# Kernel optimization log

Hardware: AMD Instinct MI355X
Metric: run time of the kernel (lower is better)

The kernel has to match this reference:

```python
import jax, jax.numpy as jnp
import numpy as np
from jax import lax
from jax.scipy.special import logsumexp

B, S, V, D, DFF, H, T, L = 64, 512, 30000, 128, 256, 4, 9, 2
HD = D // H


def setup_inputs() -> dict:
    key = jax.random.key(0)
    ks = jax.random.split(key, 12)
    sc = 0.02
    return {
        "sentences": jax.random.randint(ks[0], (B, S), 0, V, dtype=jnp.int32),
        "tags": jax.random.randint(ks[1], (B, S), 0, T, dtype=jnp.int32),
        "emb": jax.random.normal(ks[2], (V, D), jnp.float32) * sc,
        "Wqkv": jax.random.normal(ks[3], (L, 3 * D, D), jnp.float32) * sc,
        "bqkv": jnp.zeros((L, 3 * D), jnp.float32),
        "Wo": jax.random.normal(ks[4], (L, D, D), jnp.float32) * sc,
        "bo": jnp.zeros((L, D), jnp.float32),
        "W1": jax.random.normal(ks[5], (L, DFF, D), jnp.float32) * sc,
        "b1f": jnp.zeros((L, DFF), jnp.float32),
        "W2": jax.random.normal(ks[6], (L, D, DFF), jnp.float32) * sc,
        "b2f": jnp.zeros((L, D), jnp.float32),
        "ln1g": jnp.ones((L, D), jnp.float32), "ln1b": jnp.zeros((L, D), jnp.float32),
        "ln2g": jnp.ones((L, D), jnp.float32), "ln2b": jnp.zeros((L, D), jnp.float32),
        "Wtag": jax.random.normal(ks[7], (T, D), jnp.float32) * sc,
        "btag": jnp.zeros((T,), jnp.float32),
        "trans": jax.random.normal(ks[8], (T, T), jnp.float32) * 0.1,
        "start_t": jax.random.normal(ks[9], (T,), jnp.float32),
        "end_t": jax.random.normal(ks[10], (T,), jnp.float32),
    }


def _layernorm(x, g, b, eps=1e-5):
    mu = x.mean(-1, keepdims=True)
    var = ((x - mu) ** 2).mean(-1, keepdims=True)
    return (x - mu) / jnp.sqrt(var + eps) * g + b


def _forward_core(sentences, tags, emb, Wqkv, bqkv, Wo, bo, W1, b1f, W2, b2f,
                  ln1g, ln1b, ln2g, ln2b, Wtag, btag, trans, start_t, end_t):
    emb = emb.at[0].set(0.0)  # padding_idx=0
    mask = sentences != 0  # (B,S) key-padding mask (True = real token)
    x = emb[sentences]  # (B,S,D)
    # sinusoidal positional encoding (eval mode -> dropout is identity)
    pos = jnp.arange(S, dtype=jnp.float32)[:, None]
    div = jnp.exp(jnp.arange(0, D, 2, dtype=jnp.float32) * (-np.log(10000.0) / D))
    pe = jnp.zeros((S, D), jnp.float32).at[:, 0::2].set(jnp.sin(pos * div)).at[:, 1::2].set(jnp.cos(pos * div))
    x = x + pe[None]
    key_bias = jnp.where(mask, 0.0, -1e9)[:, None, None, :]  # (B,1,1,S)
    inv_sqrt_hd = 1.0 / np.sqrt(HD)
    for l in range(L):  # post-LN TransformerEncoderLayer, relu FFN
        qkv = x @ Wqkv[l].T + bqkv[l]
        q, k, v = jnp.split(qkv, 3, axis=-1)
        q = q.reshape(B, S, H, HD)
        k = k.reshape(B, S, H, HD)
        v = v.reshape(B, S, H, HD)
        scores = jnp.einsum('bqhd,bkhd->bhqk', q, k) * inv_sqrt_hd + key_bias
        attn = jax.nn.softmax(scores, axis=-1)
        ctx = jnp.einsum('bhqk,bkhd->bqhd', attn, v).reshape(B, S, D)
        x = _layernorm(x + ctx @ Wo[l].T + bo[l], ln1g[l], ln1b[l])
        ff = jax.nn.relu(x @ W1[l].T + b1f[l]) @ W2[l].T + b2f[l]
        x = _layernorm(x + ff, ln2g[l], ln2b[l])
    emissions = x @ Wtag.T + btag  # (B,S,T)

    # CRF forward algorithm (log-partition) as a scan over time
    fv0 = start_t[None, :] + emissions[:, 0]  # (B,T)

    def step(fv, xm):
        em_t, m_t = xm  # (B,T), (B,)
        nv = logsumexp(fv[:, :, None] + trans[None, :, :] + em_t[:, None, :], axis=1)
        return jnp.where(m_t[:, None], nv, fv), None

    fv, _ = lax.scan(step, fv0, (jnp.swapaxes(emissions[:, 1:], 0, 1),
                                 jnp.swapaxes(mask[:, 1:], 0, 1)))
    fwd_score = logsumexp(fv + end_t[None, :], axis=1)  # (B,)

    # gold path score (fully vectorized)
    bidx = jnp.arange(B)
    score = start_t[tags[:, 0]] + emissions[bidx, 0, tags[:, 0]]
    tprev, tcur = tags[:, :-1], tags[:, 1:]
    trans_sc = trans[tprev, tcur]  # (B,S-1)
    emit_sc = jnp.take_along_axis(emissions[:, 1:], tcur[:, :, None], axis=2)[:, :, 0]
    score = score + jnp.sum(jnp.where(mask[:, 1:], trans_sc + emit_sc, 0.0), axis=1)
    seq_lens = mask.sum(axis=1)
    last_tags = tags[bidx, seq_lens - 1]
    score = score + end_t[last_tags]

    return jnp.mean(fwd_score - score)


def reference(sentences, tags, emb, Wqkv, bqkv, Wo, bo, W1, b1f, W2, b2f,
              ln1g, ln1b, ln2g, ln2b, Wtag, btag, trans, start_t, end_t):
    return _forward_core(sentences, tags, emb, Wqkv, bqkv, Wo, bo, W1, b1f, W2, b2f,
                         ln1g, ln1b, ln2g, ln2b, Wtag, btag, trans, start_t, end_t)
```

## Files before the change

kernel.cpp:

```cpp
#include <hip/hip_runtime.h>
#include <hip/hip_bf16.h>

#define BB   64
#define SS   512
#define DD   128
#define DFFc 256
#define HH   4
#define TT   9
#define LL   2
#define HDc  32
#define NN   (BB*SS)

#define OFF_X    0
#define OFF_Y    (NN*DD)
#define OFF_QKV  (2*NN*DD)
#define OFF_CTX  (5*NN*DD)
#define OFF_KT   (6*NN*DD)
#define OFF_EM   (7*NN*DD)
#define OFF_PART (7*NN*DD + NN*TT)

typedef __attribute__((ext_vector_type(8))) short short8;
typedef __attribute__((ext_vector_type(8))) unsigned short ushort8;
typedef __attribute__((ext_vector_type(4))) float f32x4;

__device__ __forceinline__ unsigned short f2bf(float f) {
  union { __hip_bfloat16 h; unsigned short u; } cv;
  cv.h = __float2bfloat16(f);
  return cv.u;
}
__device__ __forceinline__ float bf2f(unsigned short h) {
  return __uint_as_float(((unsigned int)h) << 16);
}

__global__ void k_embed(const int* __restrict__ sent, const float* __restrict__ emb,
                        float* __restrict__ x,
                        unsigned short* __restrict__ xh, unsigned short* __restrict__ xl) {
  int n = blockIdx.x;
  int d = threadIdx.x;
  int tok = sent[n];
  int s = n & (SS - 1);
  float e = (tok != 0) ? emb[(size_t)tok * DD + d] : 0.f;
  int i = d >> 1;
  float dv = expf((float)(2 * i) * (-9.210340371976184f / (float)DD));
  float ang = (float)s * dv;
  float pe = (d & 1) ? cosf(ang) : sinf(ang);
  float v = e + pe;
  size_t o = (size_t)n * DD + d;
  x[o] = v;
  unsigned short h = f2bf(v);
  xh[o] = h;
  xl[o] = f2bf(v - bf2f(h));
}

__global__ void k_packw(const float* __restrict__ Wqkv, const float* __restrict__ Wo,
                        const float* __restrict__ W1, const float* __restrict__ W2,
                        unsigned short* __restrict__ Wh, unsigned short* __restrict__ Wl) {
  int idx = (blockIdx.x * 256 + threadIdx.x) * 4;
  const float* src;
  int off;
  if (idx < 49152)      { src = Wqkv; off = idx; }
  else if (idx < 65536) { src = Wo;   off = idx - 49152; }
  else if (idx < 98304) { src = W1;   off = idx - 65536; }
  else                  { src = W2;   off = idx - 98304; }
  float4 v = *(const float4*)(src + off);
  unsigned short h0 = f2bf(v.x), h1 = f2bf(v.y), h2 = f2bf(v.z), h3 = f2bf(v.w);
  Wh[idx + 0] = h0; Wh[idx + 1] = h1; Wh[idx + 2] = h2; Wh[idx + 3] = h3;
  Wl[idx + 0] = f2bf(v.x - bf2f(h0));
  Wl[idx + 1] = f2bf(v.y - bf2f(h1));
  Wl[idx + 2] = f2bf(v.z - bf2f(h2));
  Wl[idx + 3] = f2bf(v.w - bf2f(h3));
}

template <int KTOT, bool RELU, bool PACKOUT>
__global__ __launch_bounds__(256) void k_bgemm(
    const unsigned short* __restrict__ Xh, const unsigned short* __restrict__ Xl,
    const unsigned short* __restrict__ Wh, const unsigned short* __restrict__ Wl,
    const float* __restrict__ bias, float* __restrict__ Y, int ldY,
    unsigned short* __restrict__ Yh, unsigned short* __restrict__ Yl,
    int ncb) {
  const int id = blockIdx.x;
  const int cb = id % ncb, rb = id / ncb;
  const int tid = threadIdx.x, w = tid >> 6, lane = tid & 63;
  const int l15 = lane & 15, kg = lane >> 4;
  const int n0 = rb * 64 + w * 16;
  const int c0 = cb * 64;
  f32x4 acc[4] = {};
  const unsigned short* xph = Xh + (size_t)(n0 + l15) * KTOT + kg * 8;
  const unsigned short* xpl = Xl + (size_t)(n0 + l15) * KTOT + kg * 8;
  #pragma unroll
  for (int ks = 0; ks < KTOT / 32; ks++) {
    short8 ah = *(const short8*)(xph + ks * 32);
    short8 al = *(const short8*)(xpl + ks * 32);
    #pragma unroll
    for (int ct = 0; ct < 4; ct++) {
      size_t wo = (size_t)(c0 + ct * 16 + l15) * KTOT + ks * 32 + kg * 8;
      short8 bh = *(const short8*)(Wh + wo);
      short8 bl = *(const short8*)(Wl + wo);
      acc[ct] = __builtin_amdgcn_mfma_f32_16x16x32_bf16(ah, bh, acc[ct], 0, 0, 0);
      acc[ct] = __builtin_amdgcn_mfma_f32_16x16x32_bf16(ah, bl, acc[ct], 0, 0, 0);
      acc[ct] = __builtin_amdgcn_mfma_f32_16x16x32_bf16(al, bh, acc[ct], 0, 0, 0);
    }
  }
  #pragma unroll
  for (int ct = 0; ct < 4; ct++) {
    int c = c0 + ct * 16 + l15;
    float bi = bias[c];
    #pragma unroll
    for (int j = 0; j < 4; j++) {
      float v = acc[ct][j] + bi;
      if (RELU) v = fmaxf(v, 0.f);
      int n = n0 + kg * 4 + j;
      if (PACKOUT) {
        unsigned short h = f2bf(v);
        Yh[(size_t)n * ldY + c] = h;
        Yl[(size_t)n * ldY + c] = f2bf(v - bf2f(h));
      } else {
        Y[(size_t)n * ldY + c] = v;
      }
    }
  }
}

template <int KTOT>
__global__ __launch_bounds__(256) void k_bgemm_ln(
    const unsigned short* __restrict__ Xh, const unsigned short* __restrict__ Xl,
    const unsigned short* __restrict__ Wh, const unsigned short* __restrict__ Wl,
    const float* __restrict__ bias, const float* __restrict__ Res,
    const float* __restrict__ gam, const float* __restrict__ bet,
    float* __restrict__ Y,
    unsigned short* __restrict__ Yh, unsigned short* __restrict__ Yl,
    int dopack) {
  const int tid = threadIdx.x, w = tid >> 6, lane = tid & 63;
  const int l15 = lane & 15, kg = lane >> 4;
  const int n0 = blockIdx.x * 64 + w * 16;
  f32x4 acc[8] = {};
  const unsigned short* xph = Xh + (size_t)(n0 + l15) * KTOT + kg * 8;
  const unsigned short* xpl = Xl + (size_t)(n0 + l15) * KTOT + kg * 8;
  #pragma unroll
  for (int ks = 0; ks < KTOT / 32; ks++) {
    short8 ah = *(const short8*)(xph + ks * 32);
    short8 al = *(const short8*)(xpl + ks * 32);
    #pragma unroll
    for (int ct = 0; ct < 8; ct++) {
      size_t wo = (size_t)(ct * 16 + l15) * KTOT + ks * 32 + kg * 8;
      short8 bh = *(const short8*)(Wh + wo);
      short8 bl = *(const short8*)(Wl + wo);
      acc[ct] = __builtin_amdgcn_mfma_f32_16x16x32_bf16(ah, bh, acc[ct], 0, 0, 0);
      acc[ct] = __builtin_amdgcn_mfma_f32_16x16x32_bf16(ah, bl, acc[ct], 0, 0, 0);
      acc[ct] = __builtin_amdgcn_mfma_f32_16x16x32_bf16(al, bh, acc[ct], 0, 0, 0);
    }
  }
  #pragma unroll
  for (int j = 0; j < 4; j++) {
    int n = n0 + kg * 4 + j;
    float v[8], s1 = 0.f, s2 = 0.f;
    #pragma unroll
    for (int ct = 0; ct < 8; ct++) {
      int c = ct * 16 + l15;
      float t = acc[ct][j] + bias[c] + Res[(size_t)n * DD + c];
      v[ct] = t;
      s1 += t;
      s2 += t * t;
    }
    #pragma unroll
    for (int off = 1; off <= 8; off <<= 1) {
      s1 += __shfl_xor(s1, off);
      s2 += __shfl_xor(s2, off);
    }
    float mu = s1 * 0.0078125f;
    float var = s2 * 0.0078125f - mu * mu;
    float rstd = rsqrtf(var + 1e-5f);
    #pragma unroll
    for (int ct = 0; ct < 8; ct++) {
      int c = ct * 16 + l15;
      float o = (v[ct] - mu) * rstd * gam[c] + bet[c];
      size_t oo = (size_t)n * DD + c;
      Y[oo] = o;
      if (dopack) {
        unsigned short h = f2bf(o);
        Yh[oo] = h;
        Yl[oo] = f2bf(o - bf2f(h));
      }
    }
  }
}

__global__ void k_pack(const float* __restrict__ qkv,
                       unsigned short* __restrict__ Kh, unsigned short* __restrict__ Vh) {
  const int st = blockIdx.x * 64;
  const int bh = blockIdx.y;
  const int b = bh >> 2, h = bh & 3;
  const int tid = threadIdx.x;
  __shared__ float tile[64][33];
  #pragma unroll
  for (int p = 0; p < 8; p++) {
    int sl = p * 8 + (tid >> 5);
    int d = tid & 31;
    const float* src = qkv + (size_t)(b * SS + st + sl) * 384 + h * 32 + d;
    Kh[(size_t)(bh * SS + st + sl) * 32 + d] = f2bf(src[128]);
    tile[sl][d] = src[256];
  }
  __syncthreads();
  int d = tid >> 3, s0 = (tid & 7) * 8;
  ushort8 vh;
  #pragma unroll
  for (int i = 0; i < 8; i++) vh[i] = f2bf(tile[s0 + i][d]);
  *(ushort8*)&Vh[(size_t)(bh * 32 + d) * SS + st + s0] = vh;
}

__global__ __launch_bounds__(256) void k_attn(const float* __restrict__ qkv,
    const unsigned short* __restrict__ Kh, const unsigned short* __restrict__ Vh,
    const int* __restrict__ sent,
    unsigned short* __restrict__ ctxh, unsigned short* __restrict__ ctxl) {
  const int id = blockIdx.x;
  const int xcd = id & 7, rem = id >> 3;
  const int qt = rem & 7;
  const int bh = xcd + 8 * (rem >> 3);
  const int b = bh >> 2, h = bh & 3;
  const int tid = threadIdx.x, w = tid >> 6, lane = tid & 63;
  const int l15 = lane & 15, kg = lane >> 4;

  __shared__ float kb_lds[512];
  __shared__ unsigned short Ph[4][16][136];
  __shared__ float l_lds[4][16];

  for (int i = tid; i < 512; i += 256)
    kb_lds[i] = (sent[b * SS + i] != 0) ? 0.f : -1e9f;
  __syncthreads();

  const int qrow = qt * 64 + w * 16 + l15;
  const float* qp = qkv + (size_t)(b * SS + qrow) * 384 + h * 32 + kg * 8;
  short8 qh;
  #pragma unroll
  for (int i = 0; i < 8; i++) qh[i] = (short)f2bf(qp[i]);

  f32x4 acc0 = {0.f, 0.f, 0.f, 0.f};
  f32x4 acc1 = {0.f, 0.f, 0.f, 0.f};
  float ls[4] = {0.f, 0.f, 0.f, 0.f};
  const float scale = 0.17677669529663687f;

  const unsigned short* KhB = Kh + (size_t)bh * SS * 32;
  const unsigned short* VhB = Vh + (size_t)bh * 32 * SS;

  for (int c = 0; c < 4; c++) {
    const int ksb = c * 128;
    f32x4 sc[8];
    #pragma unroll
    for (int t = 0; t < 8; t++) {
      short8 kh_ = *(const short8*)(KhB + (size_t)(ksb + t * 16 + l15) * 32 + kg * 8);
      f32x4 z = {0.f, 0.f, 0.f, 0.f};
      sc[t] = __builtin_amdgcn_mfma_f32_16x16x32_bf16(qh, kh_, z, 0, 0, 0);
    }
    #pragma unroll
    for (int t = 0; t < 8; t++) {
      float kbv = kb_lds[ksb + t * 16 + l15];
      #pragma unroll
      for (int j = 0; j < 4; j++) {
        float s = fmaf(sc[t][j], scale, kbv);
        float p = __expf(s);
        ls[j] += p;
        Ph[w][kg * 4 + j][t * 16 + l15] = f2bf(p);
      }
    }
    #pragma unroll
    for (int k4 = 0; k4 < 4; k4++) {
      short8 ph_ = *(const short8*)&Ph[w][l15][k4 * 32 + kg * 8];
      short8 vh0 = *(const short8*)(VhB + (size_t)l15 * SS + ksb + k4 * 32 + kg * 8);
      short8 vh1 = *(const short8*)(VhB + (size_t)(16 + l15) * SS + ksb + k4 * 32 + kg * 8);
      acc0 = __builtin_amdgcn_mfma_f32_16x16x32_bf16(vh0, ph_, acc0, 0, 0, 0);
      acc1 = __builtin_amdgcn_mfma_f32_16x16x32_bf16(vh1, ph_, acc1, 0, 0, 0);
    }
  }
  #pragma unroll
  for (int j = 0; j < 4; j++) {
    #pragma unroll
    for (int off = 1; off <= 8; off <<= 1) ls[j] += __shfl_xor(ls[j], off);
  }
  if (l15 == 0) {
    #pragma unroll
    for (int j = 0; j < 4; j++) l_lds[w][kg * 4 + j] = ls[j];
  }
  float linv = 1.f / l_lds[w][l15];
  size_t co = (size_t)(b * SS + qrow) * DD + h * 32;
  #pragma unroll
  for (int j = 0; j < 4; j++) {
    float v0 = acc0[j] * linv;
    float v1 = acc1[j] * linv;
    unsigned short h0 = f2bf(v0), h1 = f2bf(v1);
    ctxh[co + kg * 4 + j] = h0;
    ctxl[co + kg * 4 + j] = f2bf(v0 - bf2f(h0));
    ctxh[co + 16 + kg * 4 + j] = h1;
    ctxl[co + 16 + kg * 4 + j] = f2bf(v1 - bf2f(h1));
  }
}

__global__ void k_emis(const float* __restrict__ X, const float* __restrict__ Wtag,
                       const float* __restrict__ btag, float* __restrict__ em) {
  int idx = blockIdx.x * 256 + threadIdx.x;
  if (idx >= NN * TT) return;
  int n = idx / TT, t = idx - n * TT;
  const float* xr = X + (size_t)n * DD;
  const float* wr = Wtag + (size_t)t * DD;
  float acc = 0.f;
  #pragma unroll
  for (int k = 0; k < DD / 4; k++) {
    float4 x4 = *(const float4*)(xr + 4 * k);
    float4 w4 = *(const float4*)(wr + 4 * k);
    acc += x4.x * w4.x + x4.y * w4.y + x4.z * w4.z + x4.w * w4.w;
  }
  em[idx] = acc + btag[t];
}

__global__ void k_crf_scan(const float* __restrict__ em, const int* __restrict__ sent,
                           const float* __restrict__ trans, float* __restrict__ M) {
  const int i = blockIdx.x;
  const int c = blockIdx.y;
  const int b = blockIdx.z;
  const int lane = threadIdx.x;
  const int j = (lane < TT) ? lane : 0;
  float tr[TT];
  #pragma unroll
  for (int k = 0; k < TT; k++) tr[k] = trans[k * TT + j];
  const float* emb_ = em + (size_t)b * SS * TT;
  float v = (j == i) ? 0.f : -1e30f;
  const int s0 = 1 + c * 64;
  const int s1 = (s0 + 64 < SS) ? s0 + 64 : SS;
  for (int s = s0; s < s1; s++) {
    int tok = sent[b * SS + s];
    if (tok != 0) {
      float a[TT];
      #pragma unroll
      for (int k = 0; k < TT; k++) a[k] = __shfl(v, k) + tr[k];
      float m = a[0];
      #pragma unroll
      for (int k = 1; k < TT; k++) m = fmaxf(m, a[k]);
      float sum = 0.f;
      #pragma unroll
      for (int k = 0; k < TT; k++) sum += __expf(a[k] - m);
      v = emb_[s * TT + j] + m + __logf(sum);
    }
  }
  if (lane < TT) M[(((size_t)b * 8 + c) * TT + i) * TT + j] = v;
}

__global__ void k_crf_comb(const float* __restrict__ em, const int* __restrict__ sent,
                           const int* __restrict__ tags, const float* __restrict__ trans,
                           const float* __restrict__ start_t, const float* __restrict__ end_t,
                           const float* __restrict__ M, float* __restrict__ part) {
  const int b = blockIdx.x;
  const int lane = threadIdx.x;
  const int j = (lane < TT) ? lane : 0;
  const float* emb_ = em + (size_t)b * SS * TT;
  float fv = start_t[j] + emb_[j];
  #pragma unroll
  for (int c = 0; c < 8; c++) {
    const float* Mc = M + (((size_t)b * 8 + c) * TT) * TT;
    float a[TT];
    #pragma unroll
    for (int k = 0; k < TT; k++) a[k] = __shfl(fv, k) + Mc[k * TT + j];
    float m = a[0];
    #pragma unroll
    for (int k = 1; k < TT; k++) m = fmaxf(m, a[k]);
    float sum = 0.f;
    #pragma unroll
    for (int k = 0; k < TT; k++) sum += __expf(a[k] - m);
    fv = m + __logf(sum);
  }
  float aa[TT];
  #pragma unroll
  for (int i = 0; i < TT; i++) aa[i] = __shfl(fv, i) + end_t[i];
  float m2 = aa[0];
  #pragma unroll
  for (int i = 1; i < TT; i++) m2 = fmaxf(m2, aa[i]);
  float sum2 = 0.f;
  #pragma unroll
  for (int i = 0; i < TT; i++) sum2 += __expf(aa[i] - m2);
  float fwd = m2 + __logf(sum2);
  float p = 0.f;
  int cnt = 0;
  #pragma unroll
  for (int ii = 0; ii < 8; ii++) {
    int s = lane + 64 * ii;
    cnt += (sent[b * SS + s] != 0) ? 1 : 0;
    int s2 = s + 1;
    if (s2 < SS && sent[b * SS + s2] != 0) {
      int tp = tags[b * SS + s2 - 1];
      int tc = tags[b * SS + s2];
      p += trans[tp * TT + tc] + emb_[(size_t)s2 * TT + tc];
    }
  }
  #pragma unroll
  for (int off = 32; off >= 1; off >>= 1) {
    p += __shfl_xor(p, off);
    cnt += __shfl_xor(cnt, off);
  }
  if (lane == 0) {
    int t0 = tags[b * SS];
    float score = start_t[t0] + emb_[t0] + p;
    int lastt = tags[b * SS + cnt - 1];
    score += end_t[lastt];
    part[b] = fwd - score;
  }
}

__global__ void k_final(const float* __restrict__ part, float* __restrict__ out) {
  float v = part[threadIdx.x];
  #pragma unroll
  for (int off = 32; off >= 1; off >>= 1) v += __shfl_xor(v, off);
  if (threadIdx.x == 0) out[0] = v * (1.f / 64.f);
}

extern "C" void kernel_launch(void* const* d_in, const int* in_sizes, int n_in,
                              void* d_out, int out_size, void* d_ws, size_t ws_size,
                              hipStream_t stream) {
  const int*   sent  = (const int*)d_in[0];
  const int*   tags  = (const int*)d_in[1];
  const float* emb   = (const float*)d_in[2];
  const float* Wqkv  = (const float*)d_in[3];
  const float* bqkv  = (const float*)d_in[4];
  const float* Wo    = (const float*)d_in[5];
  const float* bo    = (const float*)d_in[6];
  const float* W1    = (const float*)d_in[7];
  const float* b1f   = (const float*)d_in[8];
  const float* W2    = (const float*)d_in[9];
  const float* b2f   = (const float*)d_in[10];
  const float* ln1g  = (const float*)d_in[11];
  const float* ln1b  = (const float*)d_in[12];
  const float* ln2g  = (const float*)d_in[13];
  const float* ln2b  = (const float*)d_in[14];
  const float* Wtag  = (const float*)d_in[15];
  const float* btag  = (const float*)d_in[16];
  const float* trans = (const float*)d_in[17];
  const float* st    = (const float*)d_in[18];
  const float* et    = (const float*)d_in[19];

  float* ws   = (float*)d_ws;
  float* xA   = ws + OFF_X;
  float* xB   = ws + OFF_Y;
  float* qkv  = ws + OFF_QKV;
  float* em   = ws + OFF_EM;
  float* part = ws + OFF_PART;
  float* out  = (float*)d_out;

  unsigned short* XAh  = (unsigned short*)(ws + OFF_CTX);
  unsigned short* XAl  = XAh + (size_t)NN * DD;
  unsigned short* ctxh = XAh;
  unsigned short* ctxl = XAl;
  unsigned short* Kh   = (unsigned short*)(ws + OFF_KT);
  unsigned short* Vh   = Kh + (size_t)NN * DD;
  unsigned short* xBh  = (unsigned short*)(ws + OFF_KT);
  unsigned short* xBl  = xBh + (size_t)NN * DD;
  unsigned short* ffh  = (unsigned short*)(ws + OFF_QKV);
  unsigned short* ffl  = ffh + (size_t)NN * DFFc;
  unsigned short* Wph  = (unsigned short*)(ws + OFF_EM);
  unsigned short* Wpl  = Wph + 131072;
  float* Mbuf = ws + OFF_CTX;

  k_embed<<<NN, DD, 0, stream>>>(sent, emb, xA, XAh, XAl);

  for (int l = 0; l < LL; l++) {
    k_packw<<<128, 256, 0, stream>>>(Wqkv + (size_t)l * 3 * DD * DD,
                                     Wo + (size_t)l * DD * DD,
                                     W1 + (size_t)l * DFFc * DD,
                                     W2 + (size_t)l * DD * DFFc, Wph, Wpl);
    k_bgemm<128, false, false><<<dim3((NN / 64) * 6), 256, 0, stream>>>(
        XAh, XAl, Wph, Wpl, bqkv + l * 3 * DD, qkv, 3 * DD, nullptr, nullptr, 6);
    k_pack<<<dim3(8, BB * HH), 256, 0, stream>>>(qkv, Kh, Vh);
    k_attn<<<dim3(2048), 256, 0, stream>>>(qkv, Kh, Vh, sent, ctxh, ctxl);
    k_bgemm_ln<128><<<dim3(NN / 64), 256, 0, stream>>>(
        ctxh, ctxl, Wph + 49152, Wpl + 49152, bo + l * DD, xA,
        ln1g + l * DD, ln1b + l * DD, xB, xBh, xBl, 1);
    k_bgemm<128, true, true><<<dim3((NN / 64) * 4), 256, 0, stream>>>(
        xBh, xBl, Wph + 65536, Wpl + 65536, b1f + l * DFFc, nullptr, DFFc,
        ffh, ffl, 4);
    k_bgemm_ln<256><<<dim3(NN / 64), 256, 0, stream>>>(
        ffh, ffl, Wph + 98304, Wpl + 98304, b2f + l * DD, xB,
        ln2g + l * DD, ln2b + l * DD, xA, XAh, XAl, (l + 1 < LL) ? 1 : 0);
  }

  k_emis<<<(NN * TT + 255) / 256, 256, 0, stream>>>(xA, Wtag, btag, em);
  k_crf_scan<<<dim3(TT, 8, BB), 64, 0, stream>>>(em, sent, trans, Mbuf);
  k_crf_comb<<<BB, 64, 0, stream>>>(em, sent, tags, trans, st, et, Mbuf, part);
  k_final<<<1, 64, 0, stream>>>(part, out);
}
```

Baseline: 653.1 us.

## Fuse QKV GEMM epilogue with bf16 K/V repacking and drop pack kernel

The QKV projection now writes bf16 Q, head-major K and transposed V directly from its epilogue. This removes the fp32 qkv buffer round trip and the separate k_pack launch. Attention reads Q as bf16 vectors instead of converting fp32 on load. Block indices in the GEMMs are also remapped so that consecutive row blocks spread across XCDs. The V stores are scattered 2-byte writes with stride SS, which may be poorly coalesced.

```diff
diff --git a/kernel.cpp b/kernel.cpp
--- a/kernel.cpp
+++ b/kernel.cpp
@@ -71,6 +71,62 @@
   Wl[idx + 3] = f2bf(v.w - bf2f(h3));
 }
 
+__global__ __launch_bounds__(256) void k_bgemm_qkv(
+    const unsigned short* __restrict__ Xh, const unsigned short* __restrict__ Xl,
+    const unsigned short* __restrict__ Wh, const unsigned short* __restrict__ Wl,
+    const float* __restrict__ bias,
+    unsigned short* __restrict__ Qh, unsigned short* __restrict__ Kh,
+    unsigned short* __restrict__ Vh) {
+  const int id = blockIdx.x;
+  const int xcd = id & 7;
+  const int idx = id >> 3;
+  const int cb = idx % 6;
+  const int rb = (idx / 6) * 8 + xcd;
+  const int tid = threadIdx.x, w = tid >> 6, lane = tid & 63;
+  const int l15 = lane & 15, kg = lane >> 4;
+  const int n0 = rb * 64 + w * 16;
+  const int c0 = cb * 64;
+  f32x4 acc[4] = {};
+  const unsigned short* xph = Xh + (size_t)(n0 + l15) * DD + kg * 8;
+  const unsigned short* xpl = Xl + (size_t)(n0 + l15) * DD + kg * 8;
+  #pragma unroll
+  for (int ks = 0; ks < 4; ks++) {
+    short8 ah = *(const short8*)(xph + ks * 32);
+    short8 al = *(const short8*)(xpl + ks * 32);
+    #pragma unroll
+    for (int ct = 0; ct < 4; ct++) {
+      size_t wo = (size_t)(c0 + ct * 16 + l15) * DD + ks * 32 + kg * 8;
+      short8 bh = *(const short8*)(Wh + wo);
+      short8 bl = *(const short8*)(Wl + wo);
+      acc[ct] = __builtin_amdgcn_mfma_f32_16x16x32_bf16(ah, bh, acc[ct], 0, 0, 0);
+      acc[ct] = __builtin_amdgcn_mfma_f32_16x16x32_bf16(ah, bl, acc[ct], 0, 0, 0);
+      acc[ct] = __builtin_amdgcn_mfma_f32_16x16x32_bf16(al, bh, acc[ct], 0, 0, 0);
+    }
+  }
+  #pragma unroll
+  for (int ct = 0; ct < 4; ct++) {
+    int c = c0 + ct * 16 + l15;
+    float bi = bias[c];
+    #pragma unroll
+    for (int j = 0; j < 4; j++) {
+      float v = acc[ct][j] + bi;
+      int n = n0 + kg * 4 + j;
+      unsigned short hv = f2bf(v);
+      if (cb < 2) {
+        Qh[(size_t)n * DD + c] = hv;
+      } else if (cb < 4) {
+        int cc = c - 128, h = cc >> 5, d = cc & 31;
+        int b = n >> 9, s = n & 511;
+        Kh[((size_t)(b * 4 + h) * SS + s) * 32 + d] = hv;
+      } else {
+        int cc = c - 256, h = cc >> 5, d = cc & 31;
+        int b = n >> 9, s = n & 511;
+        Vh[((size_t)(b * 4 + h) * 32 + d) * SS + s] = hv;
+      }
+    }
+  }
+}
+
 template <int KTOT, bool RELU, bool PACKOUT>
 __global__ __launch_bounds__(256) void k_bgemm(
     const unsigned short* __restrict__ Xh, const unsigned short* __restrict__ Xl,
@@ -79,7 +135,10 @@
     unsigned short* __restrict__ Yh, unsigned short* __restrict__ Yl,
     int ncb) {
   const int id = blockIdx.x;
-  const int cb = id % ncb, rb = id / ncb;
+  const int xcd = id & 7;
+  const int idx = id >> 3;
+  const int cb = idx % ncb;
+  const int rb = (idx / ncb) * 8 + xcd;
   const int tid = threadIdx.x, w = tid >> 6, lane = tid & 63;
   const int l15 = lane & 15, kg = lane >> 4;
   const int n0 = rb * 64 + w * 16;
@@ -185,30 +244,8 @@
   }
 }
 
-__global__ void k_pack(const float* __restrict__ qkv,
-                       unsigned short* __restrict__ Kh, unsigned short* __restrict__ Vh) {
-  const int st = blockIdx.x * 64;
-  const int bh = blockIdx.y;
-  const int b = bh >> 2, h = bh & 3;
-  const int tid = threadIdx.x;
-  __shared__ float tile[64][33];
-  #pragma unroll
-  for (int p = 0; p < 8; p++) {
-    int sl = p * 8 + (tid >> 5);
-    int d = tid & 31;
-    const float* src = qkv + (size_t)(b * SS + st + sl) * 384 + h * 32 + d;
-    Kh[(size_t)(bh * SS + st + sl) * 32 + d] = f2bf(src[128]);
-    tile[sl][d] = src[256];
-  }
-  __syncthreads();
-  int d = tid >> 3, s0 = (tid & 7) * 8;
-  ushort8 vh;
-  #pragma unroll
-  for (int i = 0; i < 8; i++) vh[i] = f2bf(tile[s0 + i][d]);
-  *(ushort8*)&Vh[(size_t)(bh * 32 + d) * SS + st + s0] = vh;
-}
-
-__global__ __launch_bounds__(256) void k_attn(const float* __restrict__ qkv,
+__global__ __launch_bounds__(256) void k_attn(
+    const unsigned short* __restrict__ Qh,
     const unsigned short* __restrict__ Kh, const unsigned short* __restrict__ Vh,
     const int* __restrict__ sent,
     unsigned short* __restrict__ ctxh, unsigned short* __restrict__ ctxl) {
@@ -229,10 +266,7 @@
   __syncthreads();
 
   const int qrow = qt * 64 + w * 16 + l15;
-  const float* qp = qkv + (size_t)(b * SS + qrow) * 384 + h * 32 + kg * 8;
-  short8 qh;
-  #pragma unroll
-  for (int i = 0; i < 8; i++) qh[i] = (short)f2bf(qp[i]);
+  short8 qh = *(const short8*)(Qh + (size_t)(b * SS + qrow) * DD + h * 32 + kg * 8);
 
   f32x4 acc0 = {0.f, 0.f, 0.f, 0.f};
   f32x4 acc1 = {0.f, 0.f, 0.f, 0.f};
@@ -437,7 +471,6 @@
   float* ws   = (float*)d_ws;
   float* xA   = ws + OFF_X;
   float* xB   = ws + OFF_Y;
-  float* qkv  = ws + OFF_QKV;
   float* em   = ws + OFF_EM;
   float* part = ws + OFF_PART;
   float* out  = (float*)d_out;
@@ -452,6 +485,8 @@
   unsigned short* xBl  = xBh + (size_t)NN * DD;
   unsigned short* ffh  = (unsigned short*)(ws + OFF_QKV);
   unsigned short* ffl  = ffh + (size_t)NN * DFFc;
+  unsigned short* Qh   = (unsigned short*)(ws + OFF_QKV + 4 * (size_t)NN * DD / 2 * 2);
+  Qh = (unsigned short*)(ws + (4 * (size_t)NN * DD));
   unsigned short* Wph  = (unsigned short*)(ws + OFF_EM);
   unsigned short* Wpl  = Wph + 131072;
   float* Mbuf = ws + OFF_CTX;
@@ -463,10 +498,9 @@
                                      Wo + (size_t)l * DD * DD,
                                      W1 + (size_t)l * DFFc * DD,
                                      W2 + (size_t)l * DD * DFFc, Wph, Wpl);
-    k_bgemm<128, false, false><<<dim3((NN / 64) * 6), 256, 0, stream>>>(
-        XAh, XAl, Wph, Wpl, bqkv + l * 3 * DD, qkv, 3 * DD, nullptr, nullptr, 6);
-    k_pack<<<dim3(8, BB * HH), 256, 0, stream>>>(qkv, Kh, Vh);
-    k_attn<<<dim3(2048), 256, 0, stream>>>(qkv, Kh, Vh, sent, ctxh, ctxl);
+    k_bgemm_qkv<<<dim3((NN / 64) * 6), 256, 0, stream>>>(
+        XAh, XAl, Wph, Wpl, bqkv + l * 3 * DD, Qh, Kh, Vh);
+    k_attn<<<dim3(2048), 256, 0, stream>>>(Qh, Kh, Vh, sent, ctxh, ctxl);
     k_bgemm_ln<128><<<dim3(NN / 64), 256, 0, stream>>>(
         ctxh, ctxl, Wph + 49152, Wpl + 49152, bo + l * DD, xA,
         ln1g + l * DD, ln1b + l * DD, xB, xBh, xBl, 1);
```

Result: no change. 643.9 us (-1.4%).
